# Optimization experiments

Measured on AMD Instinct MI355X. Metric: run time of the kernel, lower is better.

## Reference

```python
import jax, jax.numpy as jnp
import numpy as np

B = 4            # num sequences
Q_LEN = 512      # new query tokens per sequence
KV_LEN = 2048    # total kv context per sequence
PAST = KV_LEN - Q_LEN
N_QO, N_KV, HEAD = 32, 8, 128
BS = 16          # page / block size
BLOCKS_PER_SEQ = KV_LEN // BS
NUM_BLOCKS = B * BLOCKS_PER_SEQ


def setup_inputs() -> dict:
    key = jax.random.key(0)
    k1, k2, k3, k4, k5 = jax.random.split(key, 5)
    n_tokens = B * Q_LEN
    query = jax.random.normal(k1, (n_tokens, N_QO * HEAD), dtype=jnp.float32)
    key_t = jax.random.normal(k2, (n_tokens, N_KV * HEAD), dtype=jnp.float32)
    value_t = jax.random.normal(k3, (n_tokens, N_KV * HEAD), dtype=jnp.float32)
    key_cache = jax.random.normal(k4, (NUM_BLOCKS, BS, N_KV, HEAD), dtype=jnp.float32)
    value_cache = jax.random.normal(k5, (NUM_BLOCKS, BS, N_KV, HEAD), dtype=jnp.float32)
    # block tables: a permutation of all blocks (each seq owns disjoint, shuffled pages)
    rng = np.random.default_rng(0)
    bt = rng.permutation(NUM_BLOCKS).reshape(B, BLOCKS_PER_SEQ).astype(np.int32)
    # slot indices (into flattened [num_blocks*block_size] token space) for the new tokens
    pos = np.arange(PAST, KV_LEN)                        # positions of new tokens in each seq
    slots = bt[:, pos // BS] * BS + (pos % BS)           # [B, Q_LEN]
    return {
        'query': query,
        'key': key_t,
        'value': value_t,
        'key_cache': key_cache,
        'value_cache': value_cache,
        'block_tables': jnp.asarray(bt),
        'new_cache_slots': jnp.asarray(slots.reshape(-1), dtype=jnp.int32),
    }


def reference(query, key, value, key_cache, value_cache, block_tables, new_cache_slots):
    n_tokens = query.shape[0]
    num_blocks, bs, n_kv, d = key_cache.shape
    b, blocks_per_seq = block_tables.shape
    q_len = n_tokens // b
    kv_len = blocks_per_seq * bs
    n_qo = query.shape[1] // d
    g = n_qo // n_kv  # GQA group size

    q = query.reshape(b, q_len, n_qo, d).astype(jnp.float32)
    k_new = key.reshape(n_tokens, n_kv, d)
    v_new = value.reshape(n_tokens, n_kv, d)

    # write new k/v into the paged cache at their slots (set_kv_cache)
    kc = key_cache.reshape(num_blocks * bs, n_kv, d).at[new_cache_slots].set(k_new)
    vc = value_cache.reshape(num_blocks * bs, n_kv, d).at[new_cache_slots].set(v_new)

    # per-sequence paged gather: token t of seq i lives at block_tables[i, t//bs]*bs + t%bs
    tok_idx = (block_tables[:, :, None] * bs + jnp.arange(bs, dtype=block_tables.dtype)).reshape(b, kv_len)
    k = kc[tok_idx].astype(jnp.float32)  # [b, kv_len, n_kv, d]
    v = vc[tok_idx].astype(jnp.float32)

    # GQA: query head (h*g + j) attends with kv head h (== repeat_interleave on kv heads)
    qg = q.reshape(b, q_len, n_kv, g, d)
    sm_scale = 1.0 / jnp.sqrt(jnp.float32(d))
    scores = jnp.einsum('bqhgd,bkhd->bhgqk', qg, k) * sm_scale  # [b, n_kv, g, q, kv]

    # causal mask with offset: mask where k_idx - q_idx > kv_len - q_len
    q_idx = jnp.arange(q_len)
    k_idx = jnp.arange(kv_len)
    mask = (k_idx[None, :] - q_idx[:, None]) > (kv_len - q_len)  # [q, kv]
    scores = jnp.where(mask, -jnp.inf, scores)

    p = jax.nn.softmax(scores, axis=-1)
    o = jnp.einsum('bhgqk,bkhd->bqhgd', p, v)  # [b, q, n_kv, g, d]
    return o.reshape(n_tokens, n_qo * d).astype(query.dtype)
```

## Files before the change

kernel.cpp:

```cpp
#include <hip/hip_runtime.h>
#include <hip/hip_bf16.h>

#define BQ    4
#define QL    512
#define KVL   2048
#define PASTN 1536
#define NKV   8
#define DH    128
#define BPS   128

typedef __bf16 bf16x8 __attribute__((ext_vector_type(8)));
typedef float  f32x4  __attribute__((ext_vector_type(4)));

#if __has_builtin(__builtin_amdgcn_exp2f)
#define EXP2F(x) __builtin_amdgcn_exp2f(x)
#else
#define EXP2F(x) exp2f(x)
#endif

__device__ __forceinline__ unsigned short f32_to_bf16(float f) {
    unsigned u = __builtin_bit_cast(unsigned, f);
    u += 0x7fffu + ((u >> 16) & 1u);
    return (unsigned short)(u >> 16);
}

__device__ __forceinline__ unsigned pk_bf16(float a, float b) {
    return (unsigned)f32_to_bf16(a) | ((unsigned)f32_to_bf16(b) << 16);
}

__device__ __forceinline__ unsigned pk_trunc(float lo, float hi) {
    return __builtin_amdgcn_perm(__builtin_bit_cast(unsigned, hi),
                                 __builtin_bit_cast(unsigned, lo), 0x07060302u);
}

__device__ __forceinline__ void load_lds16(const unsigned short* g, unsigned short* l) {
    __builtin_amdgcn_global_load_lds(
        (const __attribute__((address_space(1))) void*)g,
        (__attribute__((address_space(3))) void*)l, 16, 0, 0);
}

__global__ __launch_bounds__(256) void gather_k_kernel(
    const float* __restrict__ key, const float* __restrict__ key_cache,
    const int* __restrict__ bt, unsigned short* __restrict__ Kb)
{
  const int gidx = blockIdx.x * 256 + threadIdx.x;
  const int d  = (gidx & 31) * 4;
  const int p  = (gidx >> 5) & (KVL - 1);
  const int bh = gidx >> 16;
  const int hh = bh & 7;
  const int bb = bh >> 3;
  const float* src;
  if (p < PASTN) {
    const int blk = bt[bb * BPS + (p >> 4)];
    src = key_cache + (size_t)((blk * 16 + (p & 15)) * 8 + hh) * DH + d;
  } else {
    src = key + (size_t)((bb * QL + (p - PASTN)) * 8 + hh) * DH + d;
  }
  const float4 v = *(const float4*)src;
  uint2 o;
  o.x = pk_bf16(v.x, v.y);
  o.y = pk_bf16(v.z, v.w);
  *(uint2*)(Kb + ((size_t)bh * KVL + p) * DH + d) = o;
}

#define VLS 132
__global__ __launch_bounds__(256) void gather_vt_kernel(
    const float* __restrict__ value, const float* __restrict__ value_cache,
    const int* __restrict__ bt, unsigned short* __restrict__ VTb)
{
  __shared__ unsigned short Vl[64 * VLS];
  const int t   = blockIdx.x & 31;
  const int hh  = (blockIdx.x >> 5) & 7;
  const int bb  = blockIdx.x >> 8;
  const int tid = threadIdx.x;
  const int dl  = (tid & 31) * 4;
  const int p0  = tid >> 5;
#pragma unroll
  for (int it = 0; it < 8; ++it) {
    const int pl = p0 + it * 8;
    const int gp = t * 64 + pl;
    const float* src;
    if (gp < PASTN) {
      const int blk = bt[bb * BPS + (gp >> 4)];
      src = value_cache + (size_t)((blk * 16 + (gp & 15)) * 8 + hh) * DH + dl;
    } else {
      src = value + (size_t)((bb * QL + (gp - PASTN)) * 8 + hh) * DH + dl;
    }
    const float4 v = *(const float4*)src;
    uint2 o;
    o.x = pk_bf16(v.x, v.y);
    o.y = pk_bf16(v.z, v.w);
    *(uint2*)&Vl[pl * VLS + dl] = o;
  }
  __syncthreads();
#pragma unroll
  for (int it = 0; it < 4; ++it) {
    const int slot = it * 256 + tid;
    const int d    = slot >> 3;
    const int kv0  = (slot & 7) * 8;
    unsigned rr[4];
#pragma unroll
    for (int i = 0; i < 4; ++i) {
      const unsigned lo = Vl[(kv0 + 2 * i) * VLS + d];
      const unsigned hi = Vl[(kv0 + 2 * i + 1) * VLS + d];
      rr[i] = lo | (hi << 16);
    }
    *(uint4*)(VTb + ((size_t)(bb * 8 + hh) * DH + d) * KVL + t * 64 + kv0) =
        make_uint4(rr[0], rr[1], rr[2], rr[3]);
  }
}

__global__ __launch_bounds__(512, 4) void attn_kernel(
    const float* __restrict__ query,
    const unsigned short* __restrict__ Kb,
    const unsigned short* __restrict__ VTb,
    float* __restrict__ out)
{
  __shared__ unsigned short Klds[2][64 * 128];
  __shared__ unsigned short Vtlds[2][128 * 64];
  __shared__ unsigned short Pw[8][16 * 40];

  const int tid  = threadIdx.x;
  const int w    = tid >> 6;
  const int lane = tid & 63;
  const int c    = lane & 15;
  const int a    = lane >> 4;
  const int hw   = w & 3;
  const int qs   = w >> 2;

  const int gid = blockIdx.x;
  const int qb  = gid >> 5;
  const int bh  = gid & 31;
  const int b   = bh >> 3;
  const int h   = bh & 7;
  const int q0  = qb * 32;
  const int n_tiles = ((PASTN + q0 + 31) >> 6) + 1;
  const int limw = PASTN + q0 + 16 * qs - 64 * (n_tiles - 1);
  const int hq  = h * 4 + hw;

  const float qscale = 0.08838834764831845f * 1.4426950408889634f;

  bf16x8 qf[4];
  {
    const float* qp = query + (size_t)(b * QL + q0 + 16 * qs + c) * 4096 + hq * DH + a * 8;
#pragma unroll
    for (int ks = 0; ks < 4; ++ks) {
      float4 x = *(const float4*)(qp + ks * 32);
      float4 y = *(const float4*)(qp + ks * 32 + 4);
      uint4 u;
      u.x = pk_bf16(x.x * qscale, x.y * qscale);
      u.y = pk_bf16(x.z * qscale, x.w * qscale);
      u.z = pk_bf16(y.x * qscale, y.y * qscale);
      u.w = pk_bf16(y.z * qscale, y.w * qscale);
      qf[ks] = __builtin_bit_cast(bf16x8, u);
    }
  }

  bf16x8 vones;
#pragma unroll
  for (int i = 0; i < 8; ++i) vones[i] = (__bf16)1.0f;

  f32x4 Oacc[8];
#pragma unroll
  for (int dt = 0; dt < 8; ++dt) Oacc[dt] = (f32x4){0.f, 0.f, 0.f, 0.f};
  f32x4 Lacc = (f32x4){0.f, 0.f, 0.f, 0.f};

  const int swz = (c & 7) << 3;

  const int krow0 = 8 * w + (lane >> 4);
  const int krow1 = krow0 + 4;
  const int kc0 = ((((lane & 15) << 4) ^ ((krow0 & 7) << 4))) >> 1;
  const int kc1 = ((((lane & 15) << 4) ^ ((krow1 & 7) << 4))) >> 1;
  const unsigned short* kgp0 = Kb + ((size_t)bh * KVL + krow0) * DH + kc0;
  const unsigned short* kgp1 = Kb + ((size_t)bh * KVL + krow1) * DH + kc1;
  const int vrow0 = 16 * w + (lane >> 3);
  const int vrow1 = vrow0 + 8;
  const int vc0 = ((((lane & 7) << 4) ^ ((vrow0 & 7) << 4))) >> 1;
  const int vc1 = ((((lane & 7) << 4) ^ ((vrow1 & 7) << 4))) >> 1;
  const unsigned short* vgp0 = VTb + ((size_t)bh * DH + vrow0) * KVL + vc0;
  const unsigned short* vgp1 = VTb + ((size_t)bh * DH + vrow1) * KVL + vc1;

  auto issue_tile = [&](int buf) {
    load_lds16(kgp0, &Klds[buf][(2 * w) * 512]);
    load_lds16(kgp1, &Klds[buf][(2 * w + 1) * 512]);
    load_lds16(vgp0, &Vtlds[buf][(2 * w) * 512]);
    load_lds16(vgp1, &Vtlds[buf][(2 * w + 1) * 512]);
    kgp0 += 64 * DH; kgp1 += 64 * DH;
    vgp0 += 64;      vgp1 += 64;
  };

  issue_tile(0);

  for (int t = 0; t < n_tiles; ++t) {
    const int buf = t & 1;
    __syncthreads();
    if (t + 1 < n_tiles) issue_tile(buf ^ 1);

    f32x4 S[4];
#pragma unroll
    for (int kvt = 0; kvt < 4; ++kvt) S[kvt] = (f32x4){0.f, 0.f, 0.f, 0.f};

#pragma unroll
    for (int ks = 0; ks < 4; ++ks) {
      bf16x8 af[4];
#pragma unroll
      for (int kvt = 0; kvt < 4; ++kvt)
        af[kvt] = __builtin_bit_cast(bf16x8,
            *(const uint4*)&Klds[buf][(16 * kvt + c) * 128 + ((32 * ks + 8 * a) ^ swz)]);
#pragma unroll
      for (int kvt = 0; kvt < 4; ++kvt)
        S[kvt] = __builtin_amdgcn_mfma_f32_16x16x32_bf16(af[kvt], qf[ks], S[kvt], 0, 0, 0);
    }

    if (t == n_tiles - 1) {
#pragma unroll
      for (int kvt = 0; kvt < 4; ++kvt)
#pragma unroll
        for (int r = 0; r < 4; ++r)
          S[kvt][r] = (16 * kvt + 4 * a + r - c > limw) ? -1e30f : S[kvt][r];
    }

#pragma unroll
    for (int half = 0; half < 2; ++half) {
#pragma unroll
      for (int kk = 0; kk < 2; ++kk) {
        const int kvt = 2 * half + kk;
        uint2 pw2;
        pw2.x = pk_trunc(EXP2F(S[kvt][0]), EXP2F(S[kvt][1]));
        pw2.y = pk_trunc(EXP2F(S[kvt][2]), EXP2F(S[kvt][3]));
        *(uint2*)&Pw[w][c * 40 + 16 * kk + 4 * a] = pw2;
      }
      const bf16x8 pf = __builtin_bit_cast(bf16x8, *(const uint4*)&Pw[w][c * 40 + 8 * a]);
      Lacc = __builtin_amdgcn_mfma_f32_16x16x32_bf16(vones, pf, Lacc, 0, 0, 0);
#pragma unroll
      for (int dt = 0; dt < 8; ++dt) {
        const bf16x8 vf = __builtin_bit_cast(bf16x8,
            *(const uint4*)&Vtlds[buf][(16 * dt + c) * 64 + ((32 * half + 8 * a) ^ swz)]);
        Oacc[dt] = __builtin_amdgcn_mfma_f32_16x16x32_bf16(vf, pf, Oacc[dt], 0, 0, 0);
      }
    }
  }

  {
    const float inv = 1.0f / Lacc[0];
    float* op = out + (size_t)(b * QL + q0 + 16 * qs + c) * 4096 + hq * DH + 4 * a;
#pragma unroll
    for (int dt = 0; dt < 8; ++dt) {
      float4 o4;
      o4.x = Oacc[dt][0] * inv;
      o4.y = Oacc[dt][1] * inv;
      o4.z = Oacc[dt][2] * inv;
      o4.w = Oacc[dt][3] * inv;
      *(float4*)(op + 16 * dt) = o4;
    }
  }
}

extern "C" void kernel_launch(void* const* d_in, const int* in_sizes, int n_in,
                              void* d_out, int out_size, void* d_ws, size_t ws_size,
                              hipStream_t stream) {
  const float* query = (const float*)d_in[0];
  const float* key   = (const float*)d_in[1];
  const float* value = (const float*)d_in[2];
  const float* kc    = (const float*)d_in[3];
  const float* vc    = (const float*)d_in[4];
  const int*   bt    = (const int*)d_in[5];
  float* out = (float*)d_out;

  unsigned short* Kb  = (unsigned short*)d_ws;
  unsigned short* VTb = Kb + (size_t)32 * KVL * DH;

  gather_k_kernel<<<8192, 256, 0, stream>>>(key, kc, bt, Kb);
  gather_vt_kernel<<<1024, 256, 0, stream>>>(value, vc, bt, VTb);
  attn_kernel<<<512, 512, 0, stream>>>(query, Kb, VTb, out);
}
```

Before: 238.6 us.

## Switch attention to 32x32x16 MFMA with in-register P via permlane32 swap

Rewrites the attention kernel to use 32x32x16 bf16 MFMA tiles, so each 256-thread block handles 32 queries per head with one wave per GQA head instead of two waves of 16 queries. The probability tile is rearranged between lanes with v_permlane32_swap instead of going through an LDS staging buffer. The row sum is accumulated in scalar registers rather than by an extra MFMA against ones. This is meant to cut LDS traffic and MFMA instruction count, at the cost of fewer threads per block and higher register pressure from the 16-wide accumulators.

```diff
diff --git a/kernel.cpp b/kernel.cpp
--- a/kernel.cpp
+++ b/kernel.cpp
@@ -11,6 +11,7 @@
 
 typedef __bf16 bf16x8 __attribute__((ext_vector_type(8)));
 typedef float  f32x4  __attribute__((ext_vector_type(4)));
+typedef float  f32x16 __attribute__((ext_vector_type(16)));
 
 #if __has_builtin(__builtin_amdgcn_exp2f)
 #define EXP2F(x) __builtin_amdgcn_exp2f(x)
@@ -37,6 +38,15 @@
     __builtin_amdgcn_global_load_lds(
         (const __attribute__((address_space(1))) void*)g,
         (__attribute__((address_space(3))) void*)l, 16, 0, 0);
+}
+
+__device__ __forceinline__ void swap32(unsigned &x, unsigned &y) {
+    asm("v_permlane32_swap_b32 %0, %1" : "+v"(x), "+v"(y));
+}
+
+__device__ __forceinline__ void lacc_add(float &L, unsigned p) {
+    L += __builtin_bit_cast(float, p << 16);
+    L += __builtin_bit_cast(float, p & 0xffff0000u);
 }
 
 __global__ __launch_bounds__(256) void gather_k_kernel(
@@ -110,7 +120,7 @@
   }
 }
 
-__global__ __launch_bounds__(512, 4) void attn_kernel(
+__global__ __launch_bounds__(256, 2) void attn_kernel(
     const float* __restrict__ query,
     const unsigned short* __restrict__ Kb,
     const unsigned short* __restrict__ VTb,
@@ -118,15 +128,13 @@
 {
   __shared__ unsigned short Klds[2][64 * 128];
   __shared__ unsigned short Vtlds[2][128 * 64];
-  __shared__ unsigned short Pw[8][16 * 40];
 
   const int tid  = threadIdx.x;
   const int w    = tid >> 6;
   const int lane = tid & 63;
-  const int c    = lane & 15;
-  const int a    = lane >> 4;
-  const int hw   = w & 3;
-  const int qs   = w >> 2;
+  const int cq   = lane & 31;
+  const int hi   = lane >> 5;
+  const int xk   = cq & 7;
 
   const int gid = blockIdx.x;
   const int qb  = gid >> 5;
@@ -135,18 +143,48 @@
   const int h   = bh & 7;
   const int q0  = qb * 32;
   const int n_tiles = ((PASTN + q0 + 31) >> 6) + 1;
-  const int limw = PASTN + q0 + 16 * qs - 64 * (n_tiles - 1);
-  const int hq  = h * 4 + hw;
+  const int lim = PASTN + q0 - 64 * (n_tiles - 1);
+  const int hq  = h * 4 + w;
+
+  const int kx = lane >> 4;
+  const int ku = lane & 15;
+  const unsigned short* kgp[4];
+#pragma unroll
+  for (int i = 0; i < 4; ++i) {
+    const int row = 16 * w + 4 * i + kx;
+    kgp[i] = Kb + ((size_t)bh * KVL + row) * DH + (ku ^ (row & 7)) * 8;
+  }
+  const int vx = lane >> 3;
+  const int vu = lane & 7;
+  const unsigned short* vgp[4];
+#pragma unroll
+  for (int i = 0; i < 4; ++i) {
+    const int row = 32 * w + 8 * i + vx;
+    vgp[i] = VTb + ((size_t)bh * DH + row) * KVL + (vu ^ vx) * 8;
+  }
+
+  auto issue_tile = [&](int buf) {
+#pragma unroll
+    for (int i = 0; i < 4; ++i)
+      load_lds16(kgp[i], &Klds[buf][2048 * w + 512 * i]);
+#pragma unroll
+    for (int i = 0; i < 4; ++i)
+      load_lds16(vgp[i], &Vtlds[buf][2048 * w + 512 * i]);
+#pragma unroll
+    for (int i = 0; i < 4; ++i) { kgp[i] += 64 * DH; vgp[i] += 64; }
+  };
+
+  issue_tile(0);
 
   const float qscale = 0.08838834764831845f * 1.4426950408889634f;
 
-  bf16x8 qf[4];
+  bf16x8 qf[8];
   {
-    const float* qp = query + (size_t)(b * QL + q0 + 16 * qs + c) * 4096 + hq * DH + a * 8;
-#pragma unroll
-    for (int ks = 0; ks < 4; ++ks) {
-      float4 x = *(const float4*)(qp + ks * 32);
-      float4 y = *(const float4*)(qp + ks * 32 + 4);
+    const float* qp = query + (size_t)(b * QL + q0 + cq) * 4096 + hq * DH + 8 * hi;
+#pragma unroll
+    for (int ks = 0; ks < 8; ++ks) {
+      float4 x = *(const float4*)(qp + 16 * ks);
+      float4 y = *(const float4*)(qp + 16 * ks + 4);
       uint4 u;
       u.x = pk_bf16(x.x * qscale, x.y * qscale);
       u.y = pk_bf16(x.z * qscale, x.w * qscale);
@@ -156,102 +194,81 @@
     }
   }
 
-  bf16x8 vones;
-#pragma unroll
-  for (int i = 0; i < 8; ++i) vones[i] = (__bf16)1.0f;
-
-  f32x4 Oacc[8];
-#pragma unroll
-  for (int dt = 0; dt < 8; ++dt) Oacc[dt] = (f32x4){0.f, 0.f, 0.f, 0.f};
-  f32x4 Lacc = (f32x4){0.f, 0.f, 0.f, 0.f};
-
-  const int swz = (c & 7) << 3;
-
-  const int krow0 = 8 * w + (lane >> 4);
-  const int krow1 = krow0 + 4;
-  const int kc0 = ((((lane & 15) << 4) ^ ((krow0 & 7) << 4))) >> 1;
-  const int kc1 = ((((lane & 15) << 4) ^ ((krow1 & 7) << 4))) >> 1;
-  const unsigned short* kgp0 = Kb + ((size_t)bh * KVL + krow0) * DH + kc0;
-  const unsigned short* kgp1 = Kb + ((size_t)bh * KVL + krow1) * DH + kc1;
-  const int vrow0 = 16 * w + (lane >> 3);
-  const int vrow1 = vrow0 + 8;
-  const int vc0 = ((((lane & 7) << 4) ^ ((vrow0 & 7) << 4))) >> 1;
-  const int vc1 = ((((lane & 7) << 4) ^ ((vrow1 & 7) << 4))) >> 1;
-  const unsigned short* vgp0 = VTb + ((size_t)bh * DH + vrow0) * KVL + vc0;
-  const unsigned short* vgp1 = VTb + ((size_t)bh * DH + vrow1) * KVL + vc1;
-
-  auto issue_tile = [&](int buf) {
-    load_lds16(kgp0, &Klds[buf][(2 * w) * 512]);
-    load_lds16(kgp1, &Klds[buf][(2 * w + 1) * 512]);
-    load_lds16(vgp0, &Vtlds[buf][(2 * w) * 512]);
-    load_lds16(vgp1, &Vtlds[buf][(2 * w + 1) * 512]);
-    kgp0 += 64 * DH; kgp1 += 64 * DH;
-    vgp0 += 64;      vgp1 += 64;
-  };
-
-  issue_tile(0);
+  f32x16 Oacc[4];
+#pragma unroll
+  for (int dt = 0; dt < 4; ++dt)
+#pragma unroll
+    for (int i = 0; i < 16; ++i) Oacc[dt][i] = 0.f;
+  float Ls = 0.f;
 
   for (int t = 0; t < n_tiles; ++t) {
     const int buf = t & 1;
     __syncthreads();
     if (t + 1 < n_tiles) issue_tile(buf ^ 1);
 
-    f32x4 S[4];
-#pragma unroll
-    for (int kvt = 0; kvt < 4; ++kvt) S[kvt] = (f32x4){0.f, 0.f, 0.f, 0.f};
-
-#pragma unroll
-    for (int ks = 0; ks < 4; ++ks) {
-      bf16x8 af[4];
-#pragma unroll
-      for (int kvt = 0; kvt < 4; ++kvt)
-        af[kvt] = __builtin_bit_cast(bf16x8,
-            *(const uint4*)&Klds[buf][(16 * kvt + c) * 128 + ((32 * ks + 8 * a) ^ swz)]);
-#pragma unroll
-      for (int kvt = 0; kvt < 4; ++kvt)
-        S[kvt] = __builtin_amdgcn_mfma_f32_16x16x32_bf16(af[kvt], qf[ks], S[kvt], 0, 0, 0);
+    f32x16 S0, S1;
+#pragma unroll
+    for (int i = 0; i < 16; ++i) { S0[i] = 0.f; S1[i] = 0.f; }
+#pragma unroll
+    for (int ks = 0; ks < 8; ++ks) {
+      const bf16x8 a0 = __builtin_bit_cast(bf16x8,
+          *(const uint4*)&Klds[buf][(cq)      * 128 + 8 * ((2 * ks + hi) ^ xk)]);
+      const bf16x8 a1 = __builtin_bit_cast(bf16x8,
+          *(const uint4*)&Klds[buf][(32 + cq) * 128 + 8 * ((2 * ks + hi) ^ xk)]);
+      S0 = __builtin_amdgcn_mfma_f32_32x32x16_bf16(a0, qf[ks], S0, 0, 0, 0);
+      S1 = __builtin_amdgcn_mfma_f32_32x32x16_bf16(a1, qf[ks], S1, 0, 0, 0);
     }
 
     if (t == n_tiles - 1) {
 #pragma unroll
-      for (int kvt = 0; kvt < 4; ++kvt)
-#pragma unroll
-        for (int r = 0; r < 4; ++r)
-          S[kvt][r] = (16 * kvt + 4 * a + r - c > limw) ? -1e30f : S[kvt][r];
-    }
-
-#pragma unroll
-    for (int half = 0; half < 2; ++half) {
-#pragma unroll
-      for (int kk = 0; kk < 2; ++kk) {
-        const int kvt = 2 * half + kk;
-        uint2 pw2;
-        pw2.x = pk_trunc(EXP2F(S[kvt][0]), EXP2F(S[kvt][1]));
-        pw2.y = pk_trunc(EXP2F(S[kvt][2]), EXP2F(S[kvt][3]));
-        *(uint2*)&Pw[w][c * 40 + 16 * kk + 4 * a] = pw2;
+      for (int reg = 0; reg < 16; ++reg) {
+        const int rr = (reg & 3) + 8 * (reg >> 2) + 4 * hi;
+        if (rr - cq > lim)      S0[reg] = -1e30f;
+        if (32 + rr - cq > lim) S1[reg] = -1e30f;
       }
-      const bf16x8 pf = __builtin_bit_cast(bf16x8, *(const uint4*)&Pw[w][c * 40 + 8 * a]);
-      Lacc = __builtin_amdgcn_mfma_f32_16x16x32_bf16(vones, pf, Lacc, 0, 0, 0);
-#pragma unroll
-      for (int dt = 0; dt < 8; ++dt) {
-        const bf16x8 vf = __builtin_bit_cast(bf16x8,
-            *(const uint4*)&Vtlds[buf][(16 * dt + c) * 64 + ((32 * half + 8 * a) ^ swz)]);
-        Oacc[dt] = __builtin_amdgcn_mfma_f32_16x16x32_bf16(vf, pf, Oacc[dt], 0, 0, 0);
+    }
+
+    auto do_half = [&](const f32x16 &S, int kvt) {
+#pragma unroll
+      for (int s = 0; s < 2; ++s) {
+        unsigned p01 = pk_trunc(EXP2F(S[8 * s + 0]), EXP2F(S[8 * s + 1]));
+        unsigned p23 = pk_trunc(EXP2F(S[8 * s + 2]), EXP2F(S[8 * s + 3]));
+        unsigned q01 = pk_trunc(EXP2F(S[8 * s + 4]), EXP2F(S[8 * s + 5]));
+        unsigned q23 = pk_trunc(EXP2F(S[8 * s + 6]), EXP2F(S[8 * s + 7]));
+        lacc_add(Ls, p01); lacc_add(Ls, p23);
+        lacc_add(Ls, q01); lacc_add(Ls, q23);
+        swap32(p01, q01);
+        swap32(p23, q23);
+        uint4 u; u.x = p01; u.y = p23; u.z = q01; u.w = q23;
+        const bf16x8 pf = __builtin_bit_cast(bf16x8, u);
+        const int ss = 2 * kvt + s;
+#pragma unroll
+        for (int dt = 0; dt < 4; ++dt) {
+          const bf16x8 vf = __builtin_bit_cast(bf16x8,
+              *(const uint4*)&Vtlds[buf][(32 * dt + cq) * 64 + 8 * ((2 * ss + hi) ^ xk)]);
+          Oacc[dt] = __builtin_amdgcn_mfma_f32_32x32x16_bf16(vf, pf, Oacc[dt], 0, 0, 0);
+        }
       }
-    }
+    };
+    do_half(S0, 0);
+    do_half(S1, 1);
   }
 
   {
-    const float inv = 1.0f / Lacc[0];
-    float* op = out + (size_t)(b * QL + q0 + 16 * qs + c) * 4096 + hq * DH + 4 * a;
-#pragma unroll
-    for (int dt = 0; dt < 8; ++dt) {
-      float4 o4;
-      o4.x = Oacc[dt][0] * inv;
-      o4.y = Oacc[dt][1] * inv;
-      o4.z = Oacc[dt][2] * inv;
-      o4.w = Oacc[dt][3] * inv;
-      *(float4*)(op + 16 * dt) = o4;
+    const float other = __shfl_xor(Ls, 32, 64);
+    const float inv = 1.0f / (Ls + other);
+    float* op = out + (size_t)(b * QL + q0 + cq) * 4096 + hq * DH + 4 * hi;
+#pragma unroll
+    for (int dt = 0; dt < 4; ++dt) {
+#pragma unroll
+      for (int rq = 0; rq < 4; ++rq) {
+        float4 o4;
+        o4.x = Oacc[dt][4 * rq + 0] * inv;
+        o4.y = Oacc[dt][4 * rq + 1] * inv;
+        o4.z = Oacc[dt][4 * rq + 2] * inv;
+        o4.w = Oacc[dt][4 * rq + 3] * inv;
+        *(float4*)(op + 32 * dt + 8 * rq) = o4;
+      }
     }
   }
 }
@@ -272,5 +289,5 @@
 
   gather_k_kernel<<<8192, 256, 0, stream>>>(key, kc, bt, Kb);
   gather_vt_kernel<<<1024, 256, 0, stream>>>(value, vc, bt, VTb);
-  attn_kernel<<<512, 512, 0, stream>>>(query, Kb, VTb, out);
-}
+  attn_kernel<<<512, 256, 0, stream>>>(query, Kb, VTb, out);
+}
```

Result: faster. 229.4 us (-3.9%).
